# Kernel tuning notes

Measured on AMD Instinct MI355X. Metric: run time of the kernel, lower is better.

## Reference

```python
import jax, jax.numpy as jnp
import numpy as np

N_INPUT = 2
N_NODES = 4
C = 64          # channel width of every state
B, H, W = 64, 32, 32
N_EDGES = sum(N_INPUT + i for i in range(N_NODES))  # 2+3+4+5 = 14


def conv1x1(x, w):
    # x: [B,C,H,W], w: [C_out,C_in] -> [B,C_out,H,W]
    return jnp.einsum('bchw,oc->bohw', x, w)


def setup_inputs() -> dict:
    key = jax.random.key(0)
    k0, k1, k2, k3 = jax.random.split(key, 4)
    x0 = jax.random.normal(k0, (B, C, H, W), dtype=jnp.float32)
    x1 = jax.random.normal(k1, (B, C, H, W), dtype=jnp.float32)
    # preproc: one 1x1 conv per input state
    W_pre = jax.random.normal(k2, (N_INPUT, C, C), dtype=jnp.float32) * (1.0 / np.sqrt(C))
    # one 1x1 conv per DAG edge (flattened in enumeration order)
    W_edge = jax.random.normal(k3, (N_EDGES, C, C), dtype=jnp.float32) * (1.0 / np.sqrt(C))
    return {'x0': x0, 'x1': x1, 'W_pre': W_pre, 'W_edge': W_edge}


def reference(x0, x1, W_pre, W_edge):
    # preprocess inputs -> initial states
    states = [conv1x1(x0, W_pre[0]), conv1x1(x1, W_pre[1])]
    e = 0
    for i in range(N_NODES):
        n_states = N_INPUT + i
        # gather every prior state, apply edge op (ReLU -> 1x1 conv), sum-merge
        s_cur = conv1x1(jax.nn.relu(states[0]), W_edge[e])
        for s in range(1, n_states):
            s_cur = s_cur + conv1x1(jax.nn.relu(states[s]), W_edge[e + s])
        e += n_states
        states.append(s_cur)
    # merger_out: concat intermediate node states (start=n_input) on channels
    return jnp.concatenate(states[N_INPUT:], axis=1)  # [B, N_NODES*C, H, W]
```

## Files before the change

### kernel.cpp

```cpp
#include <hip/hip_runtime.h>


typedef _Float16 f16;
typedef _Float16 f16x8 __attribute__((ext_vector_type(8)));
typedef float    f32x4 __attribute__((ext_vector_type(4)));

#define RSH 72
#define SB  (64 * RSH)

__device__ __forceinline__ unsigned int pkrtz(float a, float b) {
    __fp16 h2 __attribute__((ext_vector_type(2))) = __builtin_amdgcn_cvt_pkrtz(a, b);
    return __builtin_bit_cast(unsigned int, h2);
}

__global__ __launch_bounds__(256) void wconv_kernel(
    const float* __restrict__ Wpre, const float* __restrict__ Wedge,
    f16* __restrict__ ws)
{
    const int u   = blockIdx.x * 256 + threadIdx.x;
    const int k   = u >> 9;
    const int rem = u & 511;
    const int g   = rem >> 6;
    const int row = rem & 63;
    const float* src = ((k < 2) ? (Wpre + k * 4096) : (Wedge + (k - 2) * 4096))
                       + row * 64 + (g >> 2) * 32 + (g & 3) * 8;
    float4 v0 = ((const float4*)src)[0];
    float4 v1 = ((const float4*)src)[1];
    ((uint4*)ws)[u] = make_uint4(pkrtz(v0.x, v0.y), pkrtz(v0.z, v0.w),
                                 pkrtz(v1.x, v1.y), pkrtz(v1.z, v1.w));
}

__global__ __launch_bounds__(256, 3) void dag_kernel(
    const float* __restrict__ x0, const float* __restrict__ x1,
    const f16* __restrict__ wf, float* __restrict__ out)
{
    __shared__ __align__(16) f16 lds[5 * SB];

    const int t    = threadIdx.x;
    const int lane = t & 63;
    const int wv   = t >> 6;
    const int pl   = lane & 15;
    const int q    = lane >> 4;

    const int blk = blockIdx.x;
    const int b   = blk >> 4;
    const int hw0 = (blk & 15) * 64;

    const float* xg[2] = { x0 + b * 65536 + hw0, x1 + b * 65536 + hw0 };
    float* outg = out + b * 262144 + hw0;

    const f16* wl = wf + q * 512 + pl * 8;

    f16x8 wA[2][2][4];
    #pragma unroll
    for (int kb = 0; kb < 2; ++kb)
        #pragma unroll
        for (int i = 0; i < 4; ++i)
            wA[0][kb][i] = *(const f16x8*)(wl + kb * 2048 + i * 128);

    {
        const int p = t & 63, cg = t >> 6;
        #pragma unroll
        for (int inp = 0; inp < 2; ++inp) {
            const float* src = xg[inp] + (cg * 16) * 1024 + p;
            unsigned int u[8];
            #pragma unroll
            for (int i = 0; i < 8; ++i)
                u[i] = pkrtz(src[(2 * i) * 1024], src[(2 * i + 1) * 1024]);
            f16* dst = lds + (3 + inp) * SB + p * RSH + cg * 16;
            ((uint4*)dst)[0] = make_uint4(u[0], u[1], u[2], u[3]);
            ((uint4*)dst)[1] = make_uint4(u[4], u[5], u[6], u[7]);
        }
    }
    __syncthreads();

    f32x4 acc[4] = {};

    #pragma unroll
    for (int k = 0; k < 16; ++k) {
        const int src_tab[16] = { 3,4, 0,1, 0,1,2, 0,1,2,3, 0,1,2,3,4 };
        const int dst_tab[16] = { 0,1, -1,2, -1,-1,3, -1,-1,-1,4, -1,-1,-1,-1,-1 };
        const int out_tab[16] = { -1,-1, -1,0, -1,-1,1, -1,-1,-1,2, -1,-1,-1,-1,3 };
        const int cur = k & 1, nxt = cur ^ 1;

        if (k < 15) {
            const f16* wn = wl + (k + 1) * 4096;
            #pragma unroll
            for (int kb = 0; kb < 2; ++kb)
                #pragma unroll
                for (int i = 0; i < 4; ++i)
                    wA[nxt][kb][i] = *(const f16x8*)(wn + kb * 2048 + i * 128);
        }

        const f16* S = lds + src_tab[k] * SB + (wv * 16 + pl) * RSH;
        f16x8 bf[2];
        #pragma unroll
        for (int kb = 0; kb < 2; ++kb)
            bf[kb] = *(const f16x8*)(S + kb * 32 + q * 8);

        #pragma unroll
        for (int kb = 0; kb < 2; ++kb)
            #pragma unroll
            for (int i = 0; i < 4; ++i)
                acc[i] = __builtin_amdgcn_mfma_f32_16x16x32_f16(
                             wA[cur][kb][i], bf[kb], acc[i], 0, 0, 0);

        if (out_tab[k] >= 0) {
            const int p = wv * 16 + pl;
            #pragma unroll
            for (int i = 0; i < 4; ++i) {
                const int c = i * 16 + q * 4;
                #pragma unroll
                for (int r = 0; r < 4; ++r)
                    outg[(out_tab[k] * 64 + c + r) * 1024 + p] = acc[i][r];
            }
        }
        if (dst_tab[k] >= 0) {
            f16* D = lds + dst_tab[k] * SB + (wv * 16 + pl) * RSH;
            #pragma unroll
            for (int i = 0; i < 4; ++i) {
                unsigned int u0 = pkrtz(fmaxf(acc[i][0], 0.f), fmaxf(acc[i][1], 0.f));
                unsigned int u1 = pkrtz(fmaxf(acc[i][2], 0.f), fmaxf(acc[i][3], 0.f));
                *(uint2*)(D + i * 16 + q * 4) = make_uint2(u0, u1);
            }
            #pragma unroll
            for (int i = 0; i < 4; ++i) acc[i] = (f32x4){0.f, 0.f, 0.f, 0.f};
        }
    }
}

extern "C" void kernel_launch(void* const* d_in, const int* in_sizes, int n_in,
                              void* d_out, int out_size, void* d_ws, size_t ws_size,
                              hipStream_t stream) {
    const float* x0    = (const float*)d_in[0];
    const float* x1    = (const float*)d_in[1];
    const float* Wpre  = (const float*)d_in[2];
    const float* Wedge = (const float*)d_in[3];
    float* outp        = (float*)d_out;
    f16*   wfrag       = (f16*)d_ws;

    wconv_kernel<<<dim3(32), dim3(256), 0, stream>>>(Wpre, Wedge, wfrag);
    dag_kernel<<<dim3(1024), dim3(256), 0, stream>>>(x0, x1, wfrag, outp);
}
```

Baseline: 109.6 us.

## Use 2-wave blocks with 32 pixels per wave and interleave nodes 3/4 to cut LDS

Each block now runs 2 waves of 128 threads, and each wave covers 32 pixels with two accumulator sets, so every weight fragment loaded from global feeds twice as many MFMAs. The edge order is rescheduled so nodes 3 and 4 accumulate at the same time in two register sets (accA/accB). Node 3's state then overwrites the LDS slot of state 0, which brings LDS down from 5 to 4 state buffers. The cost is higher register pressure, fewer waves per block, and less latency hiding.

```diff
diff --git a/kernel.cpp b/kernel.cpp
--- a/kernel.cpp
+++ b/kernel.cpp
@@ -30,11 +30,11 @@
                                  pkrtz(v1.x, v1.y), pkrtz(v1.z, v1.w));
 }
 
-__global__ __launch_bounds__(256, 3) void dag_kernel(
+__global__ __launch_bounds__(128, 2) void dag_kernel(
     const float* __restrict__ x0, const float* __restrict__ x1,
     const f16* __restrict__ wf, float* __restrict__ out)
 {
-    __shared__ __align__(16) f16 lds[5 * SB];
+    __shared__ __align__(16) f16 lds[4 * SB];
 
     const int t    = threadIdx.x;
     const int lane = t & 63;
@@ -59,32 +59,38 @@
             wA[0][kb][i] = *(const f16x8*)(wl + kb * 2048 + i * 128);
 
     {
-        const int p = t & 63, cg = t >> 6;
+        const int p = t & 63, h = t >> 6;
         #pragma unroll
         for (int inp = 0; inp < 2; ++inp) {
-            const float* src = xg[inp] + (cg * 16) * 1024 + p;
-            unsigned int u[8];
+            const float* src = xg[inp] + (h * 32) * 1024 + p;
+            unsigned int u[16];
             #pragma unroll
-            for (int i = 0; i < 8; ++i)
+            for (int i = 0; i < 16; ++i)
                 u[i] = pkrtz(src[(2 * i) * 1024], src[(2 * i + 1) * 1024]);
-            f16* dst = lds + (3 + inp) * SB + p * RSH + cg * 16;
-            ((uint4*)dst)[0] = make_uint4(u[0], u[1], u[2], u[3]);
-            ((uint4*)dst)[1] = make_uint4(u[4], u[5], u[6], u[7]);
+            uint4* dst = (uint4*)(lds + (2 + inp) * SB + p * RSH + h * 32);
+            dst[0] = make_uint4(u[0],  u[1],  u[2],  u[3]);
+            dst[1] = make_uint4(u[4],  u[5],  u[6],  u[7]);
+            dst[2] = make_uint4(u[8],  u[9],  u[10], u[11]);
+            dst[3] = make_uint4(u[12], u[13], u[14], u[15]);
         }
     }
     __syncthreads();
 
-    f32x4 acc[4] = {};
+    f32x4 accA[2][4] = {};
+    f32x4 accB[2][4] = {};
+
+    const int widx_tab[16] = {0,1, 2,3, 4,5,6, 7,11, 8,12, 9,13, 14, 10, 15};
+    const int src_tab [16] = {2,3, 0,1, 0,1,2, 0,0,  1,1,  2,2,  3,  3,  0};
+    const int asel_tab[16] = {0,0, 0,0, 0,0,0, 0,1,  0,1,  0,1,  1,  0,  1};
+    const int out_tab [16] = {-1,-1, -1,0, -1,-1,1, -1,-1, -1,-1, -1,-1, -1, 2, 3};
+    const int dst_tab [16] = { 0, 1, -1,2, -1,-1,3, -1,-1, -1,-1, -1,-1, -1, 0,-1};
 
     #pragma unroll
     for (int k = 0; k < 16; ++k) {
-        const int src_tab[16] = { 3,4, 0,1, 0,1,2, 0,1,2,3, 0,1,2,3,4 };
-        const int dst_tab[16] = { 0,1, -1,2, -1,-1,3, -1,-1,-1,4, -1,-1,-1,-1,-1 };
-        const int out_tab[16] = { -1,-1, -1,0, -1,-1,1, -1,-1,-1,2, -1,-1,-1,-1,3 };
         const int cur = k & 1, nxt = cur ^ 1;
 
         if (k < 15) {
-            const f16* wn = wl + (k + 1) * 4096;
+            const f16* wn = wl + widx_tab[k + 1] * 4096;
             #pragma unroll
             for (int kb = 0; kb < 2; ++kb)
                 #pragma unroll
@@ -92,40 +98,65 @@
                     wA[nxt][kb][i] = *(const f16x8*)(wn + kb * 2048 + i * 128);
         }
 
-        const f16* S = lds + src_tab[k] * SB + (wv * 16 + pl) * RSH;
-        f16x8 bf[2];
+        const f16* S = lds + src_tab[k] * SB;
+        f16x8 bf[2][2];
         #pragma unroll
-        for (int kb = 0; kb < 2; ++kb)
-            bf[kb] = *(const f16x8*)(S + kb * 32 + q * 8);
+        for (int jj = 0; jj < 2; ++jj)
+            #pragma unroll
+            for (int kb = 0; kb < 2; ++kb)
+                bf[jj][kb] = *(const f16x8*)(S + (wv * 32 + jj * 16 + pl) * RSH
+                                               + kb * 32 + q * 8);
 
-        #pragma unroll
-        for (int kb = 0; kb < 2; ++kb)
+        auto step = [&](f32x4 (&acc)[2][4]) {
             #pragma unroll
-            for (int i = 0; i < 4; ++i)
-                acc[i] = __builtin_amdgcn_mfma_f32_16x16x32_f16(
-                             wA[cur][kb][i], bf[kb], acc[i], 0, 0, 0);
+            for (int jj = 0; jj < 2; ++jj)
+                #pragma unroll
+                for (int kb = 0; kb < 2; ++kb)
+                    #pragma unroll
+                    for (int i = 0; i < 4; ++i)
+                        acc[jj][i] = __builtin_amdgcn_mfma_f32_16x16x32_f16(
+                                         wA[cur][kb][i], bf[jj][kb], acc[jj][i], 0, 0, 0);
+        };
+        auto retire = [&](f32x4 (&acc)[2][4]) {
+            if (out_tab[k] >= 0) {
+                #pragma unroll
+                for (int jj = 0; jj < 2; ++jj) {
+                    const int p = wv * 32 + jj * 16 + pl;
+                    #pragma unroll
+                    for (int i = 0; i < 4; ++i) {
+                        const int c = i * 16 + q * 4;
+                        #pragma unroll
+                        for (int r = 0; r < 4; ++r)
+                            outg[(out_tab[k] * 64 + c + r) * 1024 + p] = acc[jj][i][r];
+                    }
+                }
+            }
+            if (dst_tab[k] >= 0) {
+                f16* D = lds + dst_tab[k] * SB;
+                #pragma unroll
+                for (int jj = 0; jj < 2; ++jj) {
+                    f16* Dp = D + (wv * 32 + jj * 16 + pl) * RSH;
+                    #pragma unroll
+                    for (int i = 0; i < 4; ++i) {
+                        unsigned int u0 = pkrtz(fmaxf(acc[jj][i][0], 0.f),
+                                                fmaxf(acc[jj][i][1], 0.f));
+                        unsigned int u1 = pkrtz(fmaxf(acc[jj][i][2], 0.f),
+                                                fmaxf(acc[jj][i][3], 0.f));
+                        *(uint2*)(Dp + i * 16 + q * 4) = make_uint2(u0, u1);
+                    }
+                }
+            }
+            if (out_tab[k] >= 0 || dst_tab[k] >= 0) {
+                #pragma unroll
+                for (int jj = 0; jj < 2; ++jj)
+                    #pragma unroll
+                    for (int i = 0; i < 4; ++i)
+                        acc[jj][i] = (f32x4){0.f, 0.f, 0.f, 0.f};
+            }
+        };
 
-        if (out_tab[k] >= 0) {
-            const int p = wv * 16 + pl;
-            #pragma unroll
-            for (int i = 0; i < 4; ++i) {
-                const int c = i * 16 + q * 4;
-                #pragma unroll
-                for (int r = 0; r < 4; ++r)
-                    outg[(out_tab[k] * 64 + c + r) * 1024 + p] = acc[i][r];
-            }
-        }
-        if (dst_tab[k] >= 0) {
-            f16* D = lds + dst_tab[k] * SB + (wv * 16 + pl) * RSH;
-            #pragma unroll
-            for (int i = 0; i < 4; ++i) {
-                unsigned int u0 = pkrtz(fmaxf(acc[i][0], 0.f), fmaxf(acc[i][1], 0.f));
-                unsigned int u1 = pkrtz(fmaxf(acc[i][2], 0.f), fmaxf(acc[i][3], 0.f));
-                *(uint2*)(D + i * 16 + q * 4) = make_uint2(u0, u1);
-            }
-            #pragma unroll
-            for (int i = 0; i < 4; ++i) acc[i] = (f32x4){0.f, 0.f, 0.f, 0.f};
-        }
+        if (asel_tab[k] == 0) { step(accA); retire(accA); }
+        else                  { step(accB); retire(accB); }
     }
 }
 
@@ -140,5 +171,5 @@
     f16*   wfrag       = (f16*)d_ws;
 
     wconv_kernel<<<dim3(32), dim3(256), 0, stream>>>(Wpre, Wedge, wfrag);
-    dag_kernel<<<dim3(1024), dim3(256), 0, stream>>>(x0, x1, wfrag, outp);
+    dag_kernel<<<dim3(1024), dim3(128), 0, stream>>>(x0, x1, wfrag, outp);
 }
```

After: 102.5 us. 1.07x faster.
